# Optimization experiments

Measured on AMD Instinct MI355X. Metric: run time of the kernel, lower is better.

Reference implementation:

```python
import jax, jax.numpy as jnp
import numpy as np

L, R, H, E = 2, 3, 512, 32768

def setup_inputs() -> dict:
    key = jax.random.key(0)
    ks = jax.random.split(key, 8)
    s = 1.0 / np.sqrt(H)  # keep activations sane
    return {
        "v_repr": jax.random.normal(ks[0], (E, H), jnp.float32),
        "r_repr": jax.random.normal(ks[1], (E, H), jnp.float32),
        "ent_roles": jax.random.randint(ks[2], (E,), 0, R),
        "W": jax.random.normal(ks[3], (L, R, H, H), jnp.float32) * s,
        "W_b": jnp.zeros((L, R, H), jnp.float32),
        "U": jax.random.normal(ks[4], (L, R, H, H), jnp.float32) * s,
        "U_b": jnp.zeros((L, R, H), jnp.float32),
        "P1": jax.random.normal(ks[5], (L, R, H, H), jnp.float32) * s,
        "P1_b": jnp.zeros((L, R, H), jnp.float32),
        "P2": jax.random.normal(ks[6], (L, R, H, H), jnp.float32) * s,
        "P2_b": jnp.zeros((L, R, H), jnp.float32),
        "layer_idx": 0,
    }

def reference(v_repr, r_repr, ent_roles, W, W_b, U, U_b, P1, P1_b, P2, P2_b, layer_idx):
    # Select this layer's per-role weight stacks: (R, H, H) / (R, H)
    Wl, Wbl = W[layer_idx], W_b[layer_idx]
    Ul, Ubl = U[layer_idx], U_b[layer_idx]
    P1l, P1bl = P1[layer_idx], P1_b[layer_idx]
    P2l, P2bl = P2[layer_idx], P2_b[layer_idx]
    out = jnp.zeros_like(v_repr)
    for role in range(R):  # fixed small role set
        mask = (ent_roles == role)[:, None]  # (E, 1)
        v_p = v_repr @ Wl[role].T + Wbl[role]   # nn.Linear: x @ W.T + b
        r_p = r_repr @ Ul[role].T + Ubl[role]
        h = v_p * r_p
        p = jax.nn.relu(h @ P1l[role].T + P1bl[role]) @ P2l[role].T + P2bl[role]
        out = out + jnp.where(mask, p, 0.0)
    return out
```

## Files before the change

### kernel.cpp

```cpp
#include <hip/hip_runtime.h>
#include <cstdint>
#include <cstddef>

#define E_TOT 32768
#define HD    512
#define NR    3
#define EPAD_MAX 33152
#define NTM   259
#define NB    1036
#define NB2   2072

typedef __attribute__((ext_vector_type(8))) short short8;
typedef __attribute__((ext_vector_type(4))) float f32x4;

static __device__ __forceinline__ unsigned short f2bf(float f) {
  union { float f; unsigned int u; } x; x.f = f;
  unsigned int u = x.u;
  return (unsigned short)((u + 0x7fffu + ((u >> 16) & 1u)) >> 16);
}
static __device__ __forceinline__ float bf2f(unsigned short h) {
  union { unsigned int u; float f; } x; x.u = ((unsigned int)h) << 16;
  return x.f;
}

static __device__ __forceinline__ void gload_lds16(const void* g, void* l) {
  __builtin_amdgcn_global_load_lds(
      (const __attribute__((address_space(1))) unsigned int*)g,
      (__attribute__((address_space(3))) unsigned int*)l, 16, 0, 0);
}

template <int NWG>
static __device__ __forceinline__ int chunk_swz(int bid) {
  constexpr int q = NWG / 8, r = NWG % 8;
  const int x = bid & 7, i = bid >> 3;
  return (x < r) ? x * (q + 1) + i : r * (q + 1) + (x - r) * q + i;
}


#define AL128(x) (((x) + 127) & ~127)

__global__ void k_sort1(const int* __restrict__ roles, int* __restrict__ ctrl) {
  __shared__ int cnt[NR];
  const int t = threadIdx.x;
  if (t < NR) cnt[t] = 0;
  __syncthreads();
  int c0 = 0, c1 = 0, c2 = 0;
  for (int i = t; i < E_TOT; i += 1024) {
    const int ro = roles[i];
    c0 += (ro == 0); c1 += (ro == 1); c2 += (ro == 2);
  }
  if (c0) atomicAdd(&cnt[0], c0);
  if (c1) atomicAdd(&cnt[1], c1);
  if (c2) atomicAdd(&cnt[2], c2);
  __syncthreads();
  if (t == 0) {
    const int off1 = AL128(cnt[0]);
    const int off2 = AL128(off1 + cnt[1]);
    const int ptot = AL128(off2 + cnt[2]);
    ctrl[0] = cnt[0]; ctrl[1] = cnt[1]; ctrl[2] = cnt[2];
    ctrl[4] = 0; ctrl[5] = off1; ctrl[6] = off2; ctrl[7] = ptot;
    ctrl[9] = 0; ctrl[10] = off1; ctrl[11] = off2;
  }
}

__global__ void k_scatter(const int* __restrict__ roles, int* __restrict__ ctrl,
                          int* __restrict__ perm) {
  int e = blockIdx.x * 256 + threadIdx.x;
  int lane = threadIdx.x & 63;
  int role = roles[e];
#pragma unroll
  for (int r = 0; r < NR; ++r) {
    unsigned long long m = __ballot(role == r);
    if (!m) continue;
    int leader = __ffsll((unsigned long long)m) - 1;
    int base = 0;
    if (lane == leader) base = atomicAdd(&ctrl[9 + r], (int)__popcll(m));
    base = __shfl(base, leader);
    if (role == r) {
      int rank = (int)__popcll(m & ((1ull << lane) - 1ull));
      perm[base + rank] = e;
    }
  }
}

__global__ void k_padfill(const int* __restrict__ ctrl, int* __restrict__ perm) {
#pragma unroll
  for (int r = 0; r < NR; ++r) {
    const int start = ctrl[4 + r] + ctrl[r];
    const int end = (r < 2) ? ctrl[5 + r] : EPAD_MAX;
    const int fill = (ctrl[r] > 0) ? perm[ctrl[4 + r]] : 0;
    for (int i = start + (int)threadIdx.x; i < end; i += 256) perm[i] = fill;
  }
}

__global__ void k_convw(const float* __restrict__ W, const float* __restrict__ U,
                        const float* __restrict__ P1, const float* __restrict__ P2,
                        const int* __restrict__ dlayer, short* __restrict__ dst) {
  const int per = NR * HD * HD;
  const int which = blockIdx.y;
  const float* src = (which == 0) ? W : (which == 1) ? U : (which == 2) ? P1 : P2;
  src += (size_t)dlayer[0] * per;
  short* d = dst + (size_t)which * per;
  int i = (blockIdx.x * 256 + threadIdx.x) * 4;
  if (i >= per) return;
  float4 v = *(const float4*)(src + i);
  short4 o;
  o.x = (short)f2bf(v.x); o.y = (short)f2bf(v.y);
  o.z = (short)f2bf(v.z); o.w = (short)f2bf(v.w);
  *(short4*)(d + i) = o;
}

__global__ void k_gather(const float* __restrict__ v, const float* __restrict__ r,
                         const int* __restrict__ perm,
                         short* __restrict__ vbf, short* __restrict__ rbf) {
  const int idx = blockIdx.x * 256 + threadIdx.x;
  const int row = idx >> 6;
  const int kc = (idx & 63) << 3;
  const int g = perm[row];
  const float4* pv = (const float4*)(v + (size_t)g * HD + kc);
  const float4* pr = (const float4*)(r + (size_t)g * HD + kc);
  const float4 a0 = pv[0], a1 = pv[1];
  const float4 b0 = pr[0], b1 = pr[1];
  short8 sa, sb;
#pragma unroll
  for (int j = 0; j < 4; ++j) {
    sa[j] = (short)f2bf(((const float*)&a0)[j]);
    sa[4 + j] = (short)f2bf(((const float*)&a1)[j]);
    sb[j] = (short)f2bf(((const float*)&b0)[j]);
    sb[4 + j] = (short)f2bf(((const float*)&b1)[j]);
  }
  *(short8*)(vbf + (size_t)row * HD + kc) = sa;
  *(short8*)(rbf + (size_t)row * HD + kc) = sb;
}

template <int AM, int OM, int PAIRED>
__global__ __launch_bounds__(256) void k_mm(
    const short* __restrict__ A0, const short* __restrict__ A1,
    const short* __restrict__ B0, const short* __restrict__ B1,
    const float* __restrict__ bias0, const float* __restrict__ bias1,
    const int* __restrict__ dlayer, const int* __restrict__ ctrl,
    const int* __restrict__ perm, short* __restrict__ outS0,
    short* __restrict__ outS1, float* __restrict__ outF) {
  __shared__ short As[128 * 64];
  __shared__ short Bs[128 * 64];

  int lb = chunk_swz<PAIRED ? NB2 : NB>(blockIdx.x);
  int pair = 0;
  if constexpr (PAIRED) { pair = lb >= NB ? 1 : 0; lb -= pair * NB; }
  const int m0 = (lb >> 2) * 128, n0 = (lb & 3) * 128;
  if (m0 >= ctrl[7]) return;
  const int role = (m0 >= ctrl[6]) ? 2 : (m0 >= ctrl[5] ? 1 : 0);

  const int tid = threadIdx.x;
  const int lane = tid & 63;
  const int wv = tid >> 6;
  const int wr = wv >> 1, wc = wv & 1;
  const int krow = lane & 15, ku = lane >> 4;

  const short* Brole = (PAIRED && pair ? B1 : B0) + (size_t)role * HD * HD;
  const short* Ap = (PAIRED && pair) ? A1 : A0;

  unsigned asrc[4], bsrc[4];
#pragma unroll
  for (int j = 0; j < 4; ++j) {
    const int g = j * 256 + tid;
    const int row = g >> 3;
    const int ud = (g & 7) ^ (row & 7);
    asrc[j] = (unsigned)(m0 + row) * HD + ud * 8;
    bsrc[j] = (unsigned)(n0 + row) * HD + ud * 8;
  }

  f32x4 acc[4][4];
#pragma unroll
  for (int a = 0; a < 4; ++a)
#pragma unroll
    for (int b = 0; b < 4; ++b) acc[a][b] = (f32x4)0.f;

  for (int t = 0; t < 8; ++t) {
    const int k0 = t * 64;
#pragma unroll
    for (int j = 0; j < 4; ++j)
      gload_lds16(Brole + (size_t)bsrc[j] + k0, &Bs[(j * 256 + tid) * 8]);
    if constexpr (AM == 0) {
#pragma unroll
      for (int j = 0; j < 4; ++j)
        gload_lds16(Ap + (size_t)asrc[j] + k0, &As[(j * 256 + tid) * 8]);
    } else {
#pragma unroll
      for (int j = 0; j < 4; ++j) {
        const short8 av = *(const short8*)(A0 + (size_t)asrc[j] + k0);
        const short8 ar = *(const short8*)(A1 + (size_t)asrc[j] + k0);
        short8 o;
#pragma unroll
        for (int e = 0; e < 8; ++e)
          o[e] = (short)f2bf(bf2f((unsigned short)av[e]) *
                             bf2f((unsigned short)ar[e]));
        *(short8*)&As[(j * 256 + tid) * 8] = o;
      }
    }
    __syncthreads();
    short8 fa[4][2], fb[4][2];
#pragma unroll
    for (int mi = 0; mi < 4; ++mi)
#pragma unroll
      for (int ks = 0; ks < 2; ++ks) {
        const int row = wr * 64 + mi * 16 + krow;
        fa[mi][ks] = *(const short8*)&As[row * 64 + (((ks * 4 + ku) ^ (row & 7)) * 8)];
      }
#pragma unroll
    for (int ni = 0; ni < 4; ++ni)
#pragma unroll
      for (int ks = 0; ks < 2; ++ks) {
        const int row = wc * 64 + ni * 16 + krow;
        fb[ni][ks] = *(const short8*)&Bs[row * 64 + (((ks * 4 + ku) ^ (row & 7)) * 8)];
      }
#pragma unroll
    for (int ks = 0; ks < 2; ++ks)
#pragma unroll
      for (int mi = 0; mi < 4; ++mi)
#pragma unroll
        for (int ni = 0; ni < 4; ++ni)
          acc[mi][ni] = __builtin_amdgcn_mfma_f32_16x16x32_bf16(
              fa[mi][ks], fb[ni][ks], acc[mi][ni], 0, 0, 0);
    __syncthreads();
  }

  const int ld = dlayer[0];
  const float* bias = (PAIRED && pair ? bias1 : bias0) +
                      ((size_t)ld * NR + role) * HD + n0;
  short* outS = (PAIRED && pair) ? outS1 : outS0;

  int pg[4][4];
  if constexpr (OM == 2) {
#pragma unroll
    for (int mi = 0; mi < 4; ++mi)
#pragma unroll
      for (int j = 0; j < 4; ++j)
        pg[mi][j] = perm[m0 + wr * 64 + mi * 16 + ku * 4 + j];
  }

#pragma unroll
  for (int ni = 0; ni < 4; ++ni) {
    const int col = wc * 64 + ni * 16 + krow;
    const float b = bias[col];
#pragma unroll
    for (int mi = 0; mi < 4; ++mi) {
      const int rbase = m0 + wr * 64 + mi * 16 + ku * 4;
#pragma unroll
      for (int j = 0; j < 4; ++j) {
        float val = acc[mi][ni][j] + b;
        if constexpr (OM == 0) {
          outS[(size_t)(rbase + j) * HD + n0 + col] = (short)f2bf(val);
        } else if constexpr (OM == 1) {
          val = fmaxf(val, 0.f);
          outS[(size_t)(rbase + j) * HD + n0 + col] = (short)f2bf(val);
        } else {
          outF[(size_t)pg[mi][j] * HD + n0 + col] = val;
        }
      }
    }
  }
}


extern "C" void kernel_launch(void* const* d_in, const int* in_sizes, int n_in,
                              void* d_out, int out_size, void* d_ws, size_t ws_size,
                              hipStream_t stream) {
  const float* v    = (const float*)d_in[0];
  const float* r    = (const float*)d_in[1];
  const int*   rol  = (const int*)d_in[2];
  const float* W    = (const float*)d_in[3];
  const float* Wb   = (const float*)d_in[4];
  const float* U    = (const float*)d_in[5];
  const float* Ub   = (const float*)d_in[6];
  const float* P1   = (const float*)d_in[7];
  const float* P1b  = (const float*)d_in[8];
  const float* P2   = (const float*)d_in[9];
  const float* P2b  = (const float*)d_in[10];
  const int*   dly  = (const int*)d_in[11];

  char* ws = (char*)d_ws;
  int* ctrl = (int*)ws;
  int* perm = (int*)(ws + 256);
  short* Wbf = (short*)(ws + 132864);
  short* Ubf  = Wbf + (size_t)NR * HD * HD;
  short* P1bf = Ubf + (size_t)NR * HD * HD;
  short* P2bf = P1bf + (size_t)NR * HD * HD;
  short* vbf = (short*)(ws + 6424320);
  short* rbf = vbf + (size_t)EPAD_MAX * HD;
  short* vp  = (short*)d_out;
  float* out = (float*)d_out;

  const bool bigws = ws_size >= 108267264ull;
  short* rp = bigws ? (short*)(ws + 74319616) : vbf;
  short* tb = rbf;

  k_sort1<<<1, 1024, 0, stream>>>(rol, ctrl);
  k_scatter<<<E_TOT / 256, 256, 0, stream>>>(rol, ctrl, perm);
  k_padfill<<<1, 256, 0, stream>>>(ctrl, perm);
  k_convw<<<dim3((NR * HD * HD) / 4 / 256, 4, 1), 256, 0, stream>>>(W, U, P1, P2, dly, Wbf);
  k_gather<<<EPAD_MAX * 64 / 256, 256, 0, stream>>>(v, r, perm, vbf, rbf);

  if (bigws) {
    k_mm<0, 0, 1><<<NB2, 256, 0, stream>>>(vbf, rbf, Wbf, Ubf, Wb, Ub,
                                           dly, ctrl, perm, vp, rp, nullptr);
  } else {
    k_mm<0, 0, 0><<<NB, 256, 0, stream>>>(vbf, nullptr, Wbf, nullptr, Wb, nullptr,
                                          dly, ctrl, perm, vp, nullptr, nullptr);
    k_mm<0, 0, 0><<<NB, 256, 0, stream>>>(rbf, nullptr, Ubf, nullptr, Ub, nullptr,
                                          dly, ctrl, perm, rp, nullptr, nullptr);
  }
  k_mm<1, 1, 0><<<NB, 256, 0, stream>>>(vp, rp, P1bf, nullptr, P1b, nullptr,
                                        dly, ctrl, perm, tb, nullptr, nullptr);
  k_mm<0, 2, 0><<<NB, 256, 0, stream>>>(tb, nullptr, P2bf, nullptr, P2b, nullptr,
                                        dly, ctrl, perm, nullptr, nullptr, out);

  (void)in_sizes; (void)n_in; (void)out_size;
}
```

Measured before the change: 198.7 us.

## Double-buffer LDS tiles with BK=32 to overlap global loads and MFMA

Splits the K loop into 16 steps of 32 and ping-pongs two LDS buffers, so the next tile's global-to-LDS loads are issued before the current tile's MFMAs. It uses explicit vmcnt waits and raw barriers instead of __syncthreads, and changes the XOR swizzle to suit 32-wide rows. The aim is to hide global load latency behind compute. The cost is twice as many barriers per K and hand-tuned waitcnt counts that could be wrong, causing races or stalls.

Result: no change. 201.7 us (+1.5%).

```diff
diff --git a/kernel.cpp b/kernel.cpp
--- a/kernel.cpp
+++ b/kernel.cpp
@@ -141,8 +141,8 @@
     const int* __restrict__ dlayer, const int* __restrict__ ctrl,
     const int* __restrict__ perm, short* __restrict__ outS0,
     short* __restrict__ outS1, float* __restrict__ outF) {
-  __shared__ short As[128 * 64];
-  __shared__ short Bs[128 * 64];
+  __shared__ short As[2][128 * 32];
+  __shared__ short Bs[2][128 * 32];
 
   int lb = chunk_swz<PAIRED ? NB2 : NB>(blockIdx.x);
   int pair = 0;
@@ -160,12 +160,12 @@
   const short* Brole = (PAIRED && pair ? B1 : B0) + (size_t)role * HD * HD;
   const short* Ap = (PAIRED && pair) ? A1 : A0;
 
-  unsigned asrc[4], bsrc[4];
-#pragma unroll
-  for (int j = 0; j < 4; ++j) {
+  unsigned asrc[2], bsrc[2];
+#pragma unroll
+  for (int j = 0; j < 2; ++j) {
     const int g = j * 256 + tid;
-    const int row = g >> 3;
-    const int ud = (g & 7) ^ (row & 7);
+    const int row = g >> 2;
+    const int ud = (g & 3) ^ ((row >> 1) & 3);
     asrc[j] = (unsigned)(m0 + row) * HD + ud * 8;
     bsrc[j] = (unsigned)(n0 + row) * HD + ud * 8;
   }
@@ -176,53 +176,81 @@
 #pragma unroll
     for (int b = 0; b < 4; ++b) acc[a][b] = (f32x4)0.f;
 
-  for (int t = 0; t < 8; ++t) {
-    const int k0 = t * 64;
-#pragma unroll
-    for (int j = 0; j < 4; ++j)
-      gload_lds16(Brole + (size_t)bsrc[j] + k0, &Bs[(j * 256 + tid) * 8]);
-    if constexpr (AM == 0) {
-#pragma unroll
-      for (int j = 0; j < 4; ++j)
-        gload_lds16(Ap + (size_t)asrc[j] + k0, &As[(j * 256 + tid) * 8]);
+  short8 av[2], ar[2];
+
+#define ISSUE_B(bi, K0)                                                        \
+  _Pragma("unroll") for (int j = 0; j < 2; ++j)                                \
+    gload_lds16(Brole + (size_t)bsrc[j] + (K0), &Bs[bi][(j * 256 + tid) * 8]);
+
+#define ISSUE_A(bi, K0)                                                        \
+  if constexpr (AM == 0) {                                                     \
+    _Pragma("unroll") for (int j = 0; j < 2; ++j)                              \
+      gload_lds16(Ap + (size_t)asrc[j] + (K0), &As[bi][(j * 256 + tid) * 8]);  \
+  } else {                                                                     \
+    _Pragma("unroll") for (int j = 0; j < 2; ++j) {                            \
+      av[j] = *(const short8*)(A0 + (size_t)asrc[j] + (K0));                   \
+      ar[j] = *(const short8*)(A1 + (size_t)asrc[j] + (K0));                   \
+    }                                                                          \
+  }
+
+#define WRITE_A(bi)                                                            \
+  if constexpr (AM == 1) {                                                     \
+    _Pragma("unroll") for (int j = 0; j < 2; ++j) {                            \
+      short8 o;                                                                \
+      _Pragma("unroll") for (int e = 0; e < 8; ++e)                            \
+        o[e] = (short)f2bf(bf2f((unsigned short)av[j][e]) *                    \
+                           bf2f((unsigned short)ar[j][e]));                    \
+      *(short8*)&As[bi][(j * 256 + tid) * 8] = o;                              \
+    }                                                                          \
+  }
+
+  ISSUE_B(0, 0)
+  ISSUE_A(0, 0)
+  if constexpr (AM == 1) {
+    WRITE_A(0)
+    asm volatile("s_waitcnt lgkmcnt(0)" ::: "memory");
+  }
+
+  for (int t = 0; t < 16; ++t) {
+    const int cur = t & 1, nxt = cur ^ 1;
+    if (t < 15) {
+      ISSUE_B(nxt, (t + 1) * 32)
+      ISSUE_A(nxt, (t + 1) * 32)
+    }
+    if (t < 15) {
+      if constexpr (AM == 0) asm volatile("s_waitcnt vmcnt(4)" ::: "memory");
+      else                   asm volatile("s_waitcnt vmcnt(6)" ::: "memory");
     } else {
-#pragma unroll
-      for (int j = 0; j < 4; ++j) {
-        const short8 av = *(const short8*)(A0 + (size_t)asrc[j] + k0);
-        const short8 ar = *(const short8*)(A1 + (size_t)asrc[j] + k0);
-        short8 o;
-#pragma unroll
-        for (int e = 0; e < 8; ++e)
-          o[e] = (short)f2bf(bf2f((unsigned short)av[e]) *
-                             bf2f((unsigned short)ar[e]));
-        *(short8*)&As[(j * 256 + tid) * 8] = o;
+      asm volatile("s_waitcnt vmcnt(0)" ::: "memory");
+    }
+    __builtin_amdgcn_s_barrier();
+    __builtin_amdgcn_sched_barrier(0);
+
+    short8 fa[4], fb[4];
+#pragma unroll
+    for (int mi = 0; mi < 4; ++mi) {
+      const int row = wr * 64 + mi * 16 + krow;
+      fa[mi] = *(const short8*)&As[cur][row * 32 + ((ku ^ ((row >> 1) & 3)) * 8)];
+    }
+#pragma unroll
+    for (int ni = 0; ni < 4; ++ni) {
+      const int row = wc * 64 + ni * 16 + krow;
+      fb[ni] = *(const short8*)&Bs[cur][row * 32 + ((ku ^ ((row >> 1) & 3)) * 8)];
+    }
+#pragma unroll
+    for (int mi = 0; mi < 4; ++mi)
+#pragma unroll
+      for (int ni = 0; ni < 4; ++ni)
+        acc[mi][ni] = __builtin_amdgcn_mfma_f32_16x16x32_bf16(
+            fa[mi], fb[ni], acc[mi][ni], 0, 0, 0);
+
+    if constexpr (AM == 1) {
+      if (t < 15) {
+        WRITE_A(nxt)
+        asm volatile("s_waitcnt lgkmcnt(0)" ::: "memory");
       }
     }
-    __syncthreads();
-    short8 fa[4][2], fb[4][2];
-#pragma unroll
-    for (int mi = 0; mi < 4; ++mi)
-#pragma unroll
-      for (int ks = 0; ks < 2; ++ks) {
-        const int row = wr * 64 + mi * 16 + krow;
-        fa[mi][ks] = *(const short8*)&As[row * 64 + (((ks * 4 + ku) ^ (row & 7)) * 8)];
-      }
-#pragma unroll
-    for (int ni = 0; ni < 4; ++ni)
-#pragma unroll
-      for (int ks = 0; ks < 2; ++ks) {
-        const int row = wc * 64 + ni * 16 + krow;
-        fb[ni][ks] = *(const short8*)&Bs[row * 64 + (((ks * 4 + ku) ^ (row & 7)) * 8)];
-      }
-#pragma unroll
-    for (int ks = 0; ks < 2; ++ks)
-#pragma unroll
-      for (int mi = 0; mi < 4; ++mi)
-#pragma unroll
-        for (int ni = 0; ni < 4; ++ni)
-          acc[mi][ni] = __builtin_amdgcn_mfma_f32_16x16x32_bf16(
-              fa[mi][ks], fb[ni][ks], acc[mi][ni], 0, 0, 0);
-    __syncthreads();
+    __builtin_amdgcn_s_barrier();
   }
 
   const int ld = dlayer[0];
@@ -260,6 +288,9 @@
       }
     }
   }
+#undef ISSUE_B
+#undef ISSUE_A
+#undef WRITE_A
 }
 
 
```

## Fuse row gather and bf16 conversion into first projection GEMM

Applied to the files above, without the earlier changes.

Drops the separate gather kernel that permuted v/r rows and converted them to bf16. The first paired GEMM now reads fp32 rows through the permutation index, converts them to bf16 in registers and writes them to LDS. This removes one launch and a full bf16 intermediate write and read, and frees workspace so the paired path is always used. In exchange the A operand is loaded as fp32 twice per 4 column tiles, with synchronous register loads instead of async global-to-LDS copies, so A traffic rises and latency hiding may suffer.

Result: faster. 187.4 us (-5.7%).

```diff
diff --git a/kernel.cpp b/kernel.cpp
--- a/kernel.cpp
+++ b/kernel.cpp
@@ -110,32 +110,9 @@
   *(short4*)(d + i) = o;
 }
 
-__global__ void k_gather(const float* __restrict__ v, const float* __restrict__ r,
-                         const int* __restrict__ perm,
-                         short* __restrict__ vbf, short* __restrict__ rbf) {
-  const int idx = blockIdx.x * 256 + threadIdx.x;
-  const int row = idx >> 6;
-  const int kc = (idx & 63) << 3;
-  const int g = perm[row];
-  const float4* pv = (const float4*)(v + (size_t)g * HD + kc);
-  const float4* pr = (const float4*)(r + (size_t)g * HD + kc);
-  const float4 a0 = pv[0], a1 = pv[1];
-  const float4 b0 = pr[0], b1 = pr[1];
-  short8 sa, sb;
-#pragma unroll
-  for (int j = 0; j < 4; ++j) {
-    sa[j] = (short)f2bf(((const float*)&a0)[j]);
-    sa[4 + j] = (short)f2bf(((const float*)&a1)[j]);
-    sb[j] = (short)f2bf(((const float*)&b0)[j]);
-    sb[4 + j] = (short)f2bf(((const float*)&b1)[j]);
-  }
-  *(short8*)(vbf + (size_t)row * HD + kc) = sa;
-  *(short8*)(rbf + (size_t)row * HD + kc) = sb;
-}
-
 template <int AM, int OM, int PAIRED>
 __global__ __launch_bounds__(256) void k_mm(
-    const short* __restrict__ A0, const short* __restrict__ A1,
+    const void* __restrict__ A0, const void* __restrict__ A1,
     const short* __restrict__ B0, const short* __restrict__ B1,
     const float* __restrict__ bias0, const float* __restrict__ bias1,
     const int* __restrict__ dlayer, const int* __restrict__ ctrl,
@@ -158,7 +135,8 @@
   const int krow = lane & 15, ku = lane >> 4;
 
   const short* Brole = (PAIRED && pair ? B1 : B0) + (size_t)role * HD * HD;
-  const short* Ap = (PAIRED && pair) ? A1 : A0;
+  const short* Abf = (const short*)((PAIRED && pair) ? A1 : A0);
+  const float* Af32 = (const float*)((PAIRED && pair) ? A1 : A0);
 
   unsigned asrc[4], bsrc[4];
 #pragma unroll
@@ -166,7 +144,10 @@
     const int g = j * 256 + tid;
     const int row = g >> 3;
     const int ud = (g & 7) ^ (row & 7);
-    asrc[j] = (unsigned)(m0 + row) * HD + ud * 8;
+    if constexpr (AM == 2)
+      asrc[j] = (unsigned)perm[m0 + row] * HD + ud * 8;
+    else
+      asrc[j] = (unsigned)(m0 + row) * HD + ud * 8;
     bsrc[j] = (unsigned)(n0 + row) * HD + ud * 8;
   }
 
@@ -184,17 +165,31 @@
     if constexpr (AM == 0) {
 #pragma unroll
       for (int j = 0; j < 4; ++j)
-        gload_lds16(Ap + (size_t)asrc[j] + k0, &As[(j * 256 + tid) * 8]);
-    } else {
+        gload_lds16(Abf + (size_t)asrc[j] + k0, &As[(j * 256 + tid) * 8]);
+    } else if constexpr (AM == 1) {
 #pragma unroll
       for (int j = 0; j < 4; ++j) {
-        const short8 av = *(const short8*)(A0 + (size_t)asrc[j] + k0);
-        const short8 ar = *(const short8*)(A1 + (size_t)asrc[j] + k0);
+        const short8 av = *(const short8*)((const short*)A0 + (size_t)asrc[j] + k0);
+        const short8 ar = *(const short8*)((const short*)A1 + (size_t)asrc[j] + k0);
         short8 o;
 #pragma unroll
         for (int e = 0; e < 8; ++e)
           o[e] = (short)f2bf(bf2f((unsigned short)av[e]) *
                              bf2f((unsigned short)ar[e]));
+        *(short8*)&As[(j * 256 + tid) * 8] = o;
+      }
+    } else {
+#pragma unroll
+      for (int j = 0; j < 4; ++j) {
+        const float* s = Af32 + (size_t)asrc[j] + k0;
+        const float4 x0 = *(const float4*)s;
+        const float4 x1 = *(const float4*)(s + 4);
+        short8 o;
+#pragma unroll
+        for (int e = 0; e < 4; ++e) {
+          o[e]     = (short)f2bf(((const float*)&x0)[e]);
+          o[4 + e] = (short)f2bf(((const float*)&x1)[e]);
+        }
         *(short8*)&As[(j * 256 + tid) * 8] = o;
       }
     }
@@ -286,34 +281,22 @@
   short* Ubf  = Wbf + (size_t)NR * HD * HD;
   short* P1bf = Ubf + (size_t)NR * HD * HD;
   short* P2bf = P1bf + (size_t)NR * HD * HD;
-  short* vbf = (short*)(ws + 6424320);
-  short* rbf = vbf + (size_t)EPAD_MAX * HD;
+  short* rp = (short*)(ws + 6424320);
+  short* tb = rp + (size_t)EPAD_MAX * HD;
   short* vp  = (short*)d_out;
   float* out = (float*)d_out;
-
-  const bool bigws = ws_size >= 108267264ull;
-  short* rp = bigws ? (short*)(ws + 74319616) : vbf;
-  short* tb = rbf;
 
   k_sort1<<<1, 1024, 0, stream>>>(rol, ctrl);
   k_scatter<<<E_TOT / 256, 256, 0, stream>>>(rol, ctrl, perm);
   k_padfill<<<1, 256, 0, stream>>>(ctrl, perm);
   k_convw<<<dim3((NR * HD * HD) / 4 / 256, 4, 1), 256, 0, stream>>>(W, U, P1, P2, dly, Wbf);
-  k_gather<<<EPAD_MAX * 64 / 256, 256, 0, stream>>>(v, r, perm, vbf, rbf);
-
-  if (bigws) {
-    k_mm<0, 0, 1><<<NB2, 256, 0, stream>>>(vbf, rbf, Wbf, Ubf, Wb, Ub,
-                                           dly, ctrl, perm, vp, rp, nullptr);
-  } else {
-    k_mm<0, 0, 0><<<NB, 256, 0, stream>>>(vbf, nullptr, Wbf, nullptr, Wb, nullptr,
-                                          dly, ctrl, perm, vp, nullptr, nullptr);
-    k_mm<0, 0, 0><<<NB, 256, 0, stream>>>(rbf, nullptr, Ubf, nullptr, Ub, nullptr,
-                                          dly, ctrl, perm, rp, nullptr, nullptr);
-  }
+
+  k_mm<2, 0, 1><<<NB2, 256, 0, stream>>>(v, r, Wbf, Ubf, Wb, Ub,
+                                         dly, ctrl, perm, vp, rp, nullptr);
   k_mm<1, 1, 0><<<NB, 256, 0, stream>>>(vp, rp, P1bf, nullptr, P1b, nullptr,
                                         dly, ctrl, perm, tb, nullptr, nullptr);
   k_mm<0, 2, 0><<<NB, 256, 0, stream>>>(tb, nullptr, P2bf, nullptr, P2b, nullptr,
                                         dly, ctrl, perm, nullptr, nullptr, out);
 
-  (void)in_sizes; (void)n_in; (void)out_size;
-}
+  (void)in_sizes; (void)n_in; (void)out_size; (void)ws_size;
+}
```
